# Optimization experiments

Hardware: AMD Instinct MI355X
Metric: run time of the kernel (lower is better)

## Reference

```python
import jax, jax.numpy as jnp
import numpy as np

EPS = 1e-8
SEARCH = 21  # search_window_size


def _window_stack(x, S):
    """x: [B,C,Hp,Wp] (already padded). Returns [B,C,H,W,S*S] matching
    torch unfold(2,S,1).unfold(3,S,1).reshape(...,-1) ordering (h-offset major)."""
    B, C, Hp, Wp = x.shape
    H, W = Hp - S + 1, Wp - S + 1
    patches = jax.lax.conv_general_dilated_patches(
        x, filter_shape=(S, S), window_strides=(1, 1), padding='VALID',
        dimension_numbers=('NCHW', 'OIHW', 'NCHW'))  # [B, C*S*S, H, W], (C, u, v) major->minor
    patches = patches.reshape(B, C, S * S, H, W)
    return jnp.transpose(patches, (0, 1, 3, 4, 2))  # [B,C,H,W,S*S]


def setup_inputs() -> dict:
    key = jax.random.key(0)
    k1, k2 = jax.random.split(key)
    rgb = jax.random.uniform(k1, (1, 3, 256, 256), dtype=jnp.float32)  # must be in [0,1]
    h = jnp.array([0.1], dtype=jnp.float32)  # learned NLM bandwidth parameter
    return {"rgb": rgb, "h": h}


def reference(rgb, h):
    S = SEARCH
    pad = (S - 1) // 2
    # luminance (clip only affects y, not the rgb values being averaged)
    rgb_c = jnp.clip(rgb, 0.0, 1.0)
    y = 0.299 * rgb_c[:, :1] + 0.587 * rgb_c[:, 1:2] + 0.114 * rgb_c[:, 2:]  # [B,1,H,W]

    pw = ((0, 0), (0, 0), (pad, pad), (pad, pad))
    rgb_ws = _window_stack(jnp.pad(rgb, pw, mode='reflect'), S)  # [B,3,H,W,S^2]
    y_ws = _window_stack(jnp.pad(y, pw, mode='reflect'), S)      # [B,1,H,W,S^2]

    dis = (y[..., None] - y_ws) ** 2                              # [B,1,H,W,S^2]
    dis_pad = jnp.pad(dis, ((0, 0), (0, 0), (pad, pad), (pad, pad), (0, 0)), mode='reflect')
    # sum of squared diffs over an SxS spatial window per offset (matches unfold+sum)
    dis = jax.lax.reduce_window(dis_pad, 0.0, jax.lax.add,
                                (1, 1, S, S, 1), (1, 1, 1, 1, 1), 'VALID')  # [B,1,H,W,S^2]

    distances = jnp.sqrt(jax.nn.relu(dis))
    weights = jnp.exp(-distances / (jax.nn.relu(h) + EPS))        # [B,1,H,W,S^2]
    denoised = (weights * rgb_ws).sum(-1) / weights.sum(-1)       # [B,3,H,W]
    return jnp.clip(denoised, 0.0, 1.0)
```

## Files before the change

### kernel.cpp

```cpp
#include <hip/hip_runtime.h>
#include <math.h>


#define IMG 256
#define NPIX (IMG * IMG)
#define TILE 32
#define GR 52
#define YD 72
#define YSTR 78
#define HST 54
#define NOFF 441
#define NGB 8
#define NTHR 512

typedef __attribute__((ext_vector_type(4))) _Float16 half4;
typedef __attribute__((ext_vector_type(2))) _Float16 half2_t;

#if __has_builtin(__builtin_amdgcn_fdot2)
#define FDOT2(a, b, c) __builtin_amdgcn_fdot2((a), (b), (c), false)
#else
#define FDOT2(a, b, c) ((c) + (float)(a).x * (float)(b).x + (float)(a).y * (float)(b).y)
#endif

__device__ __forceinline__ int refl(int t) {
    t = t < 0 ? -t : t;
    return t > 255 ? 510 - t : t;
}

template <bool DIRECT>
__global__ __launch_bounds__(NTHR, 4)
void nlm_main(const float* __restrict__ rgb, const float* __restrict__ hptr,
              float4* __restrict__ partials)
{
    __shared__ __align__(16) _Float16 Yreg[YD][YSTR];
    __shared__ __align__(16) _Float16 Creg4[GR][GR][4];
    __shared__ __align__(16) _Float16 hsT[8][TILE][HST];
    __shared__ unsigned char cjTab[21][GR];

    const int tid = threadIdx.x;
    const int tj = ((int)blockIdx.x & 7) * TILE;
    const int ti = ((int)blockIdx.x >> 3) * TILE;

    const int Ybi = min(max(ti - 20, 0), IMG - YD);
    const int Ybj = min(max(tj - 20, 0), IMG - YD);
    const bool interior = (ti >= 20) && (ti + 51 <= 255) && (tj >= 20) && (tj + 51 <= 255);

    for (int idx = tid; idx < YD * YD; idx += NTHR) {
        int a = idx / YD, b = idx - a * YD;
        int g = (Ybi + a) * IMG + (Ybj + b);
        float r  = fminf(fmaxf(rgb[g], 0.f), 1.f);
        float gg = fminf(fmaxf(rgb[NPIX + g], 0.f), 1.f);
        float bb = fminf(fmaxf(rgb[2 * NPIX + g], 0.f), 1.f);
        Yreg[a][b] = (_Float16)(0.299f * r + 0.587f * gg + 0.114f * bb);
    }
    for (int idx = tid; idx < GR * GR; idx += NTHR) {
        int t = idx / GR, b = idx - t * GR;
        int g = refl(ti - 10 + t) * IMG + refl(tj - 10 + b);
        half4 c;
        c.x = (_Float16)rgb[g];
        c.y = (_Float16)rgb[NPIX + g];
        c.z = (_Float16)rgb[2 * NPIX + g];
        c.w = (_Float16)1.f;
        *(half4*)&Creg4[t][b][0] = c;
    }
    if (!interior) {
        for (int idx = tid; idx < 21 * GR; idx += NTHR) {
            int d = idx / GR, c = idx - d * GR;
            cjTab[d][c] = (unsigned char)(refl(refl(tj - 10 + c) + (d - 10)) - Ybj);
        }
    }
    __syncthreads();

    const int lane = tid & 63;
    const int wv   = tid >> 6;
    const bool hact = lane < GR;

    half2_t y0h[26];
    if (hact) {
        if (interior) {
            const half2_t* q0 = (const half2_t*)&Yreg[lane + 10][10];
            #pragma unroll
            for (int i = 0; i < 26; ++i) y0h[i] = q0[i];
        } else {
            const _Float16* Y0row = &Yreg[refl(ti - 10 + lane) - Ybi][0];
            const unsigned char* cj0 = &cjTab[10][0];
            #pragma unroll
            for (int i = 0; i < 26; ++i) {
                half2_t v;
                v.x = Y0row[cj0[2 * i]];
                v.y = Y0row[cj0[2 * i + 1]];
                y0h[i] = v;
            }
        }
    }

    const float hv = fmaxf(hptr[0], 0.f);
    const float negI = -1.0f / (hv + 1e-8f);

    const int pb  = lane & 31;
    const int s16 = (lane >> 5) << 4;

    half2_t accRG[16], accBW[16];
    #pragma unroll
    for (int k = 0; k < 16; ++k) {
        accRG[k].x = (_Float16)0.f; accRG[k].y = (_Float16)0.f;
        accBW[k].x = (_Float16)0.f; accBW[k].y = (_Float16)0.f;
    }

    half2_t one; one.x = (_Float16)1.f; one.y = (_Float16)1.f;

    for (int o = (int)blockIdx.y * 8 + wv; o < NOFF; o += 64) {
        const int oq = o / 21;
        const int du = oq - 10;
        const int dv = o - oq * 21 - 10;

        if (hact) {
            const int t = lane;
            half2_t ff[26];
            if (interior) {
                if ((dv & 1) == 0) {
                    const half2_t* q1 = (const half2_t*)&Yreg[t + 10 + du][10 + dv];
                    #pragma unroll
                    for (int i = 0; i < 26; ++i) {
                        half2_t d2 = y0h[i] - q1[i];
                        ff[i] = d2 * d2;
                    }
                } else {
                    const half2_t* q1 = (const half2_t*)&Yreg[t + 10 + du][10 + dv - 1];
                    half2_t prev = q1[0];
                    #pragma unroll
                    for (int i = 0; i < 26; ++i) {
                        half2_t cur = q1[i + 1];
                        half2_t b; b.x = prev.y; b.y = cur.x;
                        half2_t d2 = y0h[i] - b;
                        ff[i] = d2 * d2;
                        prev = cur;
                    }
                }
            } else {
                const unsigned int* cw = (const unsigned int*)&cjTab[dv + 10][0];
                const _Float16* Y1row = &Yreg[refl(refl(ti - 10 + t) + du) - Ybi][0];
                #pragma unroll
                for (int i = 0; i < 26; ++i) {
                    unsigned int w0 = cw[i >> 1];
                    int sh = (i & 1) * 16;
                    _Float16 a0 = Y1row[(w0 >> sh) & 0xffu];
                    _Float16 a1 = Y1row[(w0 >> (sh + 8)) & 0xffu];
                    half2_t yv; yv.x = a0; yv.y = a1;
                    half2_t d2 = y0h[i] - yv;
                    ff[i] = d2 * d2;
                }
            }
            float s0f = 0.f, s1f = 0.f;
            #pragma unroll
            for (int i = 0; i < 10; ++i) s0f = FDOT2(ff[i], one, s0f);
            s0f += (float)ff[10].x;
            #pragma unroll
            for (int i = 8; i < 18; ++i) s1f = FDOT2(ff[i], one, s1f);
            s1f += (float)ff[18].x;
            _Float16 sA = (_Float16)s0f;
            _Float16 sB = (_Float16)s1f;
            hsT[wv][0][t]  = sA;
            hsT[wv][16][t] = sB;
            #pragma unroll
            for (int k = 1; k < 16; ++k) {
                {
                    int ja = 20 + k, jb = k - 1;
                    _Float16 fa = (ja & 1) ? ff[ja >> 1].y : ff[ja >> 1].x;
                    _Float16 fb = (jb & 1) ? ff[jb >> 1].y : ff[jb >> 1].x;
                    sA += (_Float16)(fa - fb);
                    hsT[wv][k][t] = sA;
                }
                {
                    int ja = 36 + k, jb = 15 + k;
                    _Float16 fa = (ja & 1) ? ff[ja >> 1].y : ff[ja >> 1].x;
                    _Float16 fb = (jb & 1) ? ff[jb >> 1].y : ff[jb >> 1].x;
                    sB += (_Float16)(fa - fb);
                    hsT[wv][16 + k][t] = sB;
                }
            }
        }

        {
            const half2_t* col2 = (const half2_t*)&hsT[wv][pb][s16];
            half2_t w2[18];
            #pragma unroll
            for (int i = 0; i < 18; ++i) w2[i] = col2[i];

            float vs0 = 0.f, vs1 = 0.f;
            #pragma unroll
            for (int i = 0; i < 10; ++i) vs0 = FDOT2(w2[i], one, vs0);
            vs0 += (float)w2[10].x;
            #pragma unroll
            for (int i = 4; i < 14; ++i) vs1 = FDOT2(w2[i], one, vs1);
            vs1 += (float)w2[14].x;

            float vss[16];
            vss[0] = vs0;
            vss[8] = vs1;
            #pragma unroll
            for (int k = 0; k < 7; ++k) {
                {
                    int ja = 21 + k, jb = k;
                    _Float16 fa = (ja & 1) ? w2[ja >> 1].y : w2[ja >> 1].x;
                    _Float16 fb = (jb & 1) ? w2[jb >> 1].y : w2[jb >> 1].x;
                    vss[k + 1] = vss[k] + (float)(_Float16)(fa - fb);
                }
                {
                    int ja = 29 + k, jb = 8 + k;
                    _Float16 fa = (ja & 1) ? w2[ja >> 1].y : w2[ja >> 1].x;
                    _Float16 fb = (jb & 1) ? w2[jb >> 1].y : w2[jb >> 1].x;
                    vss[k + 9] = vss[k + 8] + (float)(_Float16)(fa - fb);
                }
            }

            const int cr = s16 + 10 + du;
            const int cc = pb + 10 + dv;
            #pragma unroll
            for (int k = 0; k < 16; ++k) {
                float dist = sqrtf(fmaxf(vss[k], 0.f));
                float w = __expf(dist * negI);
                _Float16 wh = (_Float16)w;
                half2_t w2v; w2v.x = wh; w2v.y = wh;
                const half2_t* cp = (const half2_t*)&Creg4[cr + k][cc][0];
                half2_t cRG = cp[0];
                half2_t cBW = cp[1];
                accRG[k] = w2v * cRG + accRG[k];
                accBW[k] = w2v * cBW + accBW[k];
            }
        }
    }

    __syncthreads();
    float4* scratch = (float4*)&Creg4[0][0][0];
    #pragma unroll
    for (int w = 0; w < 8; ++w) {
        if (wv == w) {
            #pragma unroll
            for (int k = 0; k < 16; ++k) {
                int px = (s16 + k) * 32 + pb;
                float4 v = make_float4((float)accRG[k].x, (float)accRG[k].y,
                                       (float)accBW[k].x, (float)accBW[k].y);
                if (w == 0) scratch[px] = v;
                else {
                    float4 a = scratch[px];
                    scratch[px] = make_float4(a.x + v.x, a.y + v.y, a.z + v.z, a.w + v.w);
                }
            }
        }
        __syncthreads();
    }
    for (int i = tid; i < TILE * TILE; i += NTHR) {
        float4 v = scratch[i];
        int gpix = (ti + (i >> 5)) * IMG + (tj + (i & 31));
        if (DIRECT) {
            partials[(size_t)blockIdx.y * NPIX + gpix] = v;
        } else {
            float* p = (float*)&partials[gpix];
            atomicAdd(p + 0, v.x);
            atomicAdd(p + 1, v.y);
            atomicAdd(p + 2, v.z);
            atomicAdd(p + 3, v.w);
        }
    }
}

template <int NGT>
__global__ __launch_bounds__(256)
void nlm_finalize(const float4* __restrict__ partials, float* __restrict__ out)
{
    int idx = blockIdx.x * blockDim.x + threadIdx.x;
    float r = 0.f, g = 0.f, b = 0.f, w = 0.f;
    #pragma unroll
    for (int gg = 0; gg < NGT; ++gg) {
        float4 p = partials[(size_t)gg * NPIX + idx];
        r += p.x; g += p.y; b += p.z; w += p.w;
    }
    float inv = 1.0f / w;
    out[idx]            = fminf(fmaxf(r * inv, 0.f), 1.f);
    out[NPIX + idx]     = fminf(fmaxf(g * inv, 0.f), 1.f);
    out[2 * NPIX + idx] = fminf(fmaxf(b * inv, 0.f), 1.f);
}

extern "C" void kernel_launch(void* const* d_in, const int* in_sizes, int n_in,
                              void* d_out, int out_size, void* d_ws, size_t ws_size,
                              hipStream_t stream) {
    (void)in_sizes; (void)n_in; (void)out_size;
    const float* rgb  = (const float*)d_in[0];
    const float* hptr = (const float*)d_in[1];
    float* out = (float*)d_out;
    float4* partials = (float4*)d_ws;

    const bool direct = ws_size >= (size_t)NGB * NPIX * sizeof(float4);
    dim3 grid(64, NGB);
    if (direct) {
        nlm_main<true><<<grid, NTHR, 0, stream>>>(rgb, hptr, partials);
        nlm_finalize<NGB><<<NPIX / 256, 256, 0, stream>>>(partials, out);
    } else {
        (void)hipMemsetAsync(partials, 0, (size_t)NPIX * sizeof(float4), stream);
        nlm_main<false><<<grid, NTHR, 0, stream>>>(rgb, hptr, partials);
        nlm_finalize<1><<<NPIX / 256, 256, 0, stream>>>(partials, out);
    }
}
```

Measured before the change: 109.0 us.

## Fuse finalize into main kernel via last-block counter, simplify offset indexing

Removes the separate finalize launch in the direct path: each tile's blocks bump a global counter after writing partials, and the last of the NGB blocks sums the partials and writes the clamped output. The offset loop now steps du/dv incrementally instead of dividing by 21, and sqrtf is replaced by the raw AMDGCN sqrt builtin. This trades a kernel launch and its global pass for a memset of the counters, threadfences and a serialized tail in the last block per tile, and requires a slightly larger workspace for the direct path.

```diff
diff --git a/kernel.cpp b/kernel.cpp
--- a/kernel.cpp
+++ b/kernel.cpp
@@ -22,6 +22,12 @@
 #define FDOT2(a, b, c) ((c) + (float)(a).x * (float)(b).x + (float)(a).y * (float)(b).y)
 #endif
 
+#if __has_builtin(__builtin_amdgcn_sqrtf)
+#define ASQRT(x) __builtin_amdgcn_sqrtf(x)
+#else
+#define ASQRT(x) sqrtf(x)
+#endif
+
 __device__ __forceinline__ int refl(int t) {
     t = t < 0 ? -t : t;
     return t > 255 ? 510 - t : t;
@@ -30,12 +36,14 @@
 template <bool DIRECT>
 __global__ __launch_bounds__(NTHR, 4)
 void nlm_main(const float* __restrict__ rgb, const float* __restrict__ hptr,
-              float4* __restrict__ partials)
+              float4* __restrict__ partials, unsigned int* __restrict__ counters,
+              float* __restrict__ out)
 {
     __shared__ __align__(16) _Float16 Yreg[YD][YSTR];
     __shared__ __align__(16) _Float16 Creg4[GR][GR][4];
     __shared__ __align__(16) _Float16 hsT[8][TILE][HST];
     __shared__ unsigned char cjTab[21][GR];
+    __shared__ unsigned int doneCnt;
 
     const int tid = threadIdx.x;
     const int tj = ((int)blockIdx.x & 7) * TILE;
@@ -109,11 +117,10 @@
 
     half2_t one; one.x = (_Float16)1.f; one.y = (_Float16)1.f;
 
-    for (int o = (int)blockIdx.y * 8 + wv; o < NOFF; o += 64) {
-        const int oq = o / 21;
-        const int du = oq - 10;
-        const int dv = o - oq * 21 - 10;
-
+    const int o0 = (int)blockIdx.y * 8 + wv;
+    int du = o0 / 21 - 10;
+    int dv = o0 % 21 - 10;
+    for (int o = o0; o < NOFF; o += 64) {
         if (hact) {
             const int t = lane;
             half2_t ff[26];
@@ -218,7 +225,7 @@
             const int cc = pb + 10 + dv;
             #pragma unroll
             for (int k = 0; k < 16; ++k) {
-                float dist = sqrtf(fmaxf(vss[k], 0.f));
+                float dist = ASQRT(fmaxf(vss[k], 0.f));
                 float w = __expf(dist * negI);
                 _Float16 wh = (_Float16)w;
                 half2_t w2v; w2v.x = wh; w2v.y = wh;
@@ -229,6 +236,9 @@
                 accBW[k] = w2v * cBW + accBW[k];
             }
         }
+
+        du += 3; dv += 1;
+        if (dv > 10) { dv -= 21; du += 1; }
     }
 
     __syncthreads();
@@ -263,23 +273,39 @@
             atomicAdd(p + 3, v.w);
         }
     }
+
+    if (DIRECT) {
+        __threadfence();
+        if (tid == 0) doneCnt = atomicAdd(&counters[blockIdx.x], 1u);
+        __syncthreads();
+        if (doneCnt == NGB - 1) {
+            __threadfence();
+            for (int i = tid; i < TILE * TILE; i += NTHR) {
+                int gpix = (ti + (i >> 5)) * IMG + (tj + (i & 31));
+                float r = 0.f, g = 0.f, b = 0.f, w = 0.f;
+                #pragma unroll
+                for (int gg = 0; gg < NGB; ++gg) {
+                    float4 p = partials[(size_t)gg * NPIX + gpix];
+                    r += p.x; g += p.y; b += p.z; w += p.w;
+                }
+                float inv = 1.0f / w;
+                out[gpix]            = fminf(fmaxf(r * inv, 0.f), 1.f);
+                out[NPIX + gpix]     = fminf(fmaxf(g * inv, 0.f), 1.f);
+                out[2 * NPIX + gpix] = fminf(fmaxf(b * inv, 0.f), 1.f);
+            }
+        }
+    }
 }
 
-template <int NGT>
 __global__ __launch_bounds__(256)
-void nlm_finalize(const float4* __restrict__ partials, float* __restrict__ out)
+void nlm_finalize1(const float4* __restrict__ partials, float* __restrict__ out)
 {
     int idx = blockIdx.x * blockDim.x + threadIdx.x;
-    float r = 0.f, g = 0.f, b = 0.f, w = 0.f;
-    #pragma unroll
-    for (int gg = 0; gg < NGT; ++gg) {
-        float4 p = partials[(size_t)gg * NPIX + idx];
-        r += p.x; g += p.y; b += p.z; w += p.w;
-    }
-    float inv = 1.0f / w;
-    out[idx]            = fminf(fmaxf(r * inv, 0.f), 1.f);
-    out[NPIX + idx]     = fminf(fmaxf(g * inv, 0.f), 1.f);
-    out[2 * NPIX + idx] = fminf(fmaxf(b * inv, 0.f), 1.f);
+    float4 p = partials[idx];
+    float inv = 1.0f / p.w;
+    out[idx]            = fminf(fmaxf(p.x * inv, 0.f), 1.f);
+    out[NPIX + idx]     = fminf(fmaxf(p.y * inv, 0.f), 1.f);
+    out[2 * NPIX + idx] = fminf(fmaxf(p.z * inv, 0.f), 1.f);
 }
 
 extern "C" void kernel_launch(void* const* d_in, const int* in_sizes, int n_in,
@@ -290,15 +316,16 @@
     const float* hptr = (const float*)d_in[1];
     float* out = (float*)d_out;
     float4* partials = (float4*)d_ws;
-
-    const bool direct = ws_size >= (size_t)NGB * NPIX * sizeof(float4);
+    unsigned int* counters = (unsigned int*)((char*)d_ws + (size_t)NGB * NPIX * sizeof(float4));
+
+    const bool direct = ws_size >= (size_t)NGB * NPIX * sizeof(float4) + 4096;
     dim3 grid(64, NGB);
     if (direct) {
-        nlm_main<true><<<grid, NTHR, 0, stream>>>(rgb, hptr, partials);
-        nlm_finalize<NGB><<<NPIX / 256, 256, 0, stream>>>(partials, out);
+        (void)hipMemsetAsync(counters, 0, 64 * sizeof(unsigned int), stream);
+        nlm_main<true><<<grid, NTHR, 0, stream>>>(rgb, hptr, partials, counters, out);
     } else {
         (void)hipMemsetAsync(partials, 0, (size_t)NPIX * sizeof(float4), stream);
-        nlm_main<false><<<grid, NTHR, 0, stream>>>(rgb, hptr, partials);
-        nlm_finalize<1><<<NPIX / 256, 256, 0, stream>>>(partials, out);
+        nlm_main<false><<<grid, NTHR, 0, stream>>>(rgb, hptr, partials, counters, out);
+        nlm_finalize1<<<NPIX / 256, 256, 0, stream>>>(partials, out);
     }
 }
```

New measurement: 184.2 us. 69.0% more time.
